# Kernel optimization log

Hardware: AMD Instinct MI355X
Metric: run time of the kernel (lower is better)

## Reference

```python
import jax, jax.numpy as jnp
import numpy as np

B, N, D, H, NCB, TOPK = 4, 2048, 256, 2048, 256, 16
DP = D // 4
SCALE = float(np.sqrt(DP))
THRESH = 0.7
EPS = 1e-8


def setup_inputs() -> dict:
    key = jax.random.key(0)
    ks = jax.random.split(key, 12)
    g = lambda i, shape, s=1.0: jax.random.normal(ks[i], shape, jnp.float32) * s
    return {
        "agent_states": g(0, (B, N, D)),
        "agent_actions": g(1, (B, N, D)),
        "episodic_mem": g(2, (B, N, H)),
        "Wq": g(3, (D, DP), 0.05), "bq": jnp.zeros((DP,), jnp.float32),
        "Wk": g(4, (D, DP), 0.05), "bk": jnp.zeros((DP,), jnp.float32),
        "log_temp": jnp.asarray(0.0, jnp.float32),
        "Wc": g(5, (D, DP), 0.05), "bc": jnp.zeros((DP,), jnp.float32),
        "temp_coal": jnp.asarray(10.0, jnp.float32),
        "W_to_hdc": g(6, (D, H), 0.05), "b_to_hdc": jnp.zeros((H,), jnp.float32),
        "W_from_hdc": g(7, (H, D), 0.02), "b_from_hdc": jnp.zeros((D,), jnp.float32),
        "agent_keys": jnp.sign(g(8, (N, H))),
        "position_codes": jnp.sign(g(9, (NCB, H))),
        "step": 3,
    }


def _cosine(a, b):
    # torch F.cosine_similarity semantics, dim=-1, eps=1e-8
    na = jnp.maximum(jnp.linalg.norm(a, axis=-1), EPS)
    nb = jnp.maximum(jnp.linalg.norm(b, axis=-1), EPS)
    return jnp.sum(a * b, axis=-1) / (na * nb)


def _to_hdc_ste(x):
    soft = jnp.tanh(x * 3.0)
    hard = jnp.sign(x)
    hard = jnp.where(hard == 0, jnp.ones_like(hard), hard)
    return soft + jax.lax.stop_gradient(hard - soft)


def reference(agent_states, agent_actions, episodic_mem, Wq, bq, Wk, bk,
              log_temp, Wc, bc, temp_coal, W_to_hdc, b_to_hdc,
              W_from_hdc, b_from_hdc, agent_keys, position_codes, step):
    # ---- DynamicGraph.compute_graph: top-k dynamic attention adjacency ----
    Q = agent_actions @ Wq + bq                      # (B,N,DP)
    K = agent_actions @ Wk + bk                      # (B,N,DP)
    temp = jnp.clip(jnp.exp(log_temp), 0.1, 10.0)
    scores = jnp.einsum('bnd,bmd->bnm', Q, K) / (SCALE * temp)   # (B,N,N)
    _, topk_idx = jax.lax.top_k(scores, TOPK)                     # (B,N,k)
    bI = jnp.arange(B)[:, None, None]
    nI = jnp.arange(N)[None, :, None]
    mask = jnp.zeros_like(scores).at[bI, nI, topk_idx].set(1.0)   # scatter, like torch scatter_
    scores = scores * mask + (1.0 - mask) * -1e9
    adjacency = jax.nn.softmax(scores, axis=-1)
    # message passing over dynamic graph
    incoming = jnp.einsum('bnm,bmd->bnd', adjacency, agent_states)

    # ---- AgentCombination: sigmoid-normalized coalition mixing ----
    proj = agent_actions @ Wc + bc                   # (B,N,DP)
    pn = proj / jnp.maximum(jnp.linalg.norm(proj, axis=-1, keepdims=True), 1e-12)
    sim = jnp.einsum('bnd,bmd->bnm', pn, pn)
    cw = jax.nn.sigmoid((sim - THRESH) * temp_coal)
    cw = cw / (jnp.sum(cw, axis=-1, keepdims=True) + EPS)
    combined = jnp.einsum('bnm,bmd->bnd', cw, incoming)
    mixed = 0.8 * incoming + 0.2 * combined          # (B,N,D)

    # ---- HDCMemory: bind / write / read with STE ----
    q = _to_hdc_ste(mixed @ W_to_hdc + b_to_hdc)     # (B,N,H) bipolar via STE
    pq = q * agent_keys[None]                        # bind with agent key
    mem = jax.lax.stop_gradient(episodic_mem)        # memory read is detached in original
    pos_code = position_codes[step % NCB]            # (H,)
    new_mem = 0.95 * mem + 0.05 * (q * pos_code)     # write: bind + decay bundle
    strength = jax.nn.sigmoid(_cosine(new_mem, pq))[..., None]   # read similarity
    recall = (new_mem @ W_from_hdc + b_from_hdc) * strength      # (B,N,D)
    return mixed + recall
```

## Files before the change

kernel.cpp:

```cpp
#include <hip/hip_runtime.h>
#include <math.h>

#define BATCH 4
#define NN 2048
#define DD 256
#define HH 2048
#define DP 64
#define KTOP 16

typedef float f32x4 __attribute__((ext_vector_type(4)));
typedef short short8 __attribute__((ext_vector_type(8)));
typedef short short4v __attribute__((ext_vector_type(4)));

__device__ __forceinline__ short f2bf(float x) {
    union { float f; unsigned u; } v; v.f = x;
    unsigned r = v.u + 0x7FFFu + ((v.u >> 16) & 1u);
    return (short)(r >> 16);
}
__device__ __forceinline__ float bf2f(short s) {
    union { unsigned u; float f; } v; v.u = ((unsigned)(unsigned short)s) << 16;
    return v.f;
}

__global__ __launch_bounds__(64) void proj_kernel(
    const float* __restrict__ act,
    const float* __restrict__ Wq, const float* __restrict__ bq,
    const float* __restrict__ Wk, const float* __restrict__ bk,
    const float* __restrict__ Wc, const float* __restrict__ bc,
    float* __restrict__ Qo, float* __restrict__ Ko, short* __restrict__ Pno)
{
    const int row0 = blockIdx.x * 4;
    const int t = threadIdx.x;
    __shared__ float rowbuf[4][DD];
    const float* src = act + (size_t)row0 * DD;
    for (int i = t; i < 4 * DD; i += 64) rowbuf[i >> 8][i & 255] = src[i];
    __syncthreads();

    float q[4], k[4], c[4];
    #pragma unroll
    for (int r = 0; r < 4; ++r) { q[r] = bq[t]; k[r] = bk[t]; c[r] = bc[t]; }

    for (int d = 0; d < DD; ++d) {
        float wq = Wq[d * DP + t];
        float wk = Wk[d * DP + t];
        float wc = Wc[d * DP + t];
        #pragma unroll
        for (int r = 0; r < 4; ++r) {
            float av = rowbuf[r][d];
            q[r] = fmaf(av, wq, q[r]);
            k[r] = fmaf(av, wk, k[r]);
            c[r] = fmaf(av, wc, c[r]);
        }
    }
    #pragma unroll
    for (int r = 0; r < 4; ++r) {
        float ss = c[r] * c[r];
        #pragma unroll
        for (int off = 32; off; off >>= 1) ss += __shfl_xor(ss, off);
        float nrm = fmaxf(sqrtf(ss), 1e-12f);
        size_t o = (size_t)(row0 + r) * DP + t;
        Qo[o] = q[r];
        Ko[o] = k[r];
        Pno[o] = f2bf(c[r] / nrm);
    }
}

__global__ __launch_bounds__(256) void prep_kernel(
    const float* __restrict__ W2h, const float* __restrict__ Wfh,
    short* __restrict__ W2hT_hi, short* __restrict__ W2hT_lo,
    short* __restrict__ WfhT_hi, short* __restrict__ WfhT_lo)
{
    int b = blockIdx.x;
    const float* src; short *dhi, *dlo; int R, C, r0, c0;
    if (b < 512) {
        src = W2h; dhi = W2hT_hi; dlo = W2hT_lo; R = 256; C = 2048;
        r0 = (b >> 6) * 32; c0 = (b & 63) * 32;
    } else {
        b -= 512;
        src = Wfh; dhi = WfhT_hi; dlo = WfhT_lo; R = 2048; C = 256;
        r0 = (b >> 3) * 32; c0 = (b & 7) * 32;
    }
    int tx = threadIdx.x & 31, ty = threadIdx.x >> 5;
    __shared__ float tile[32][33];
    #pragma unroll
    for (int i = 0; i < 4; ++i)
        tile[ty + 8 * i][tx] = src[(size_t)(r0 + ty + 8 * i) * C + c0 + tx];
    __syncthreads();
    #pragma unroll
    for (int i = 0; i < 4; ++i) {
        float v = tile[tx][ty + 8 * i];
        short hi = f2bf(v);
        size_t o = (size_t)(c0 + ty + 8 * i) * R + r0 + tx;
        dhi[o] = hi;
        dlo[o] = f2bf(v - bf2f(hi));
    }
}

__global__ __launch_bounds__(512, 4) void attn_fused_kernel(
    const float* __restrict__ Q, const float* __restrict__ K,
    const float* __restrict__ log_temp,
    const float* __restrict__ states, float* __restrict__ incoming)
{
    const int t = threadIdx.x;
    const int w = t >> 6, l = t & 63;
    const int row = blockIdx.x * 8 + w;
    const int b = row >> 11;

    __shared__ float Ksh[128][68];

    const float temp = fminf(fmaxf(expf(log_temp[0]), 0.1f), 10.0f);
    const float scale = 1.0f / (8.0f * temp);

    const float* Kb = K + (size_t)b * NN * DP;
    const float4* qr4 = (const float4*)(Q + (size_t)row * DP);

    float sc[32];

    for (int ch = 0; ch < 16; ++ch) {
        __syncthreads();
        {
            int r = t >> 2, seg = t & 3;
            const float4* src = (const float4*)(Kb + (size_t)(ch * 128 + r) * DP + seg * 16);
            float4* dst = (float4*)&Ksh[r][seg * 16];
            dst[0] = src[0]; dst[1] = src[1]; dst[2] = src[2]; dst[3] = src[3];
        }
        __syncthreads();
        float a0 = 0.f, a1 = 0.f;
        const float4* k0 = (const float4*)&Ksh[l][0];
        const float4* k1 = (const float4*)&Ksh[64 + l][0];
        #pragma unroll
        for (int h = 0; h < 2; ++h) {
            float4 q[8];
            #pragma unroll
            for (int i = 0; i < 8; ++i) q[i] = qr4[h * 8 + i];
            #pragma unroll
            for (int i = 0; i < 8; ++i) {
                float4 kv0 = k0[h * 8 + i];
                float4 kv1 = k1[h * 8 + i];
                a0 = fmaf(kv0.x, q[i].x, fmaf(kv0.y, q[i].y, fmaf(kv0.z, q[i].z, fmaf(kv0.w, q[i].w, a0))));
                a1 = fmaf(kv1.x, q[i].x, fmaf(kv1.y, q[i].y, fmaf(kv1.z, q[i].z, fmaf(kv1.w, q[i].w, a1))));
            }
        }
        sc[ch * 2]     = a0 * scale;
        sc[ch * 2 + 1] = a1 * scale;
    }

    float wv = 0.f; int wm = 0;
    for (int it = 0; it < KTOP; ++it) {
        float bv = sc[0]; int bs = 0;
        #pragma unroll
        for (int i = 1; i < 32; ++i) {
            bool g = sc[i] > bv;
            bv = g ? sc[i] : bv;
            bs = g ? i : bs;
        }
        int bm = (bs >> 1) * 128 + (bs & 1) * 64 + l;
        #pragma unroll
        for (int off = 1; off < 64; off <<= 1) {
            float ov = __shfl_xor(bv, off);
            int   om = __shfl_xor(bm, off);
            bool take = (ov > bv) || (ov == bv && om < bm);
            bv = take ? ov : bv;
            bm = take ? om : bm;
        }
        if (l == it) { wv = bv; wm = bm; }
        if ((bm & 63) == l) {
            int s = ((bm >> 7) << 1) | ((bm >> 6) & 1);
            #pragma unroll
            for (int i = 0; i < 32; ++i) if (s == i) sc[i] = -3.0e38f;
        }
    }

    float mx = __shfl(wv, 0);
    float e = (l < KTOP) ? expf(wv - mx) : 0.f;
    float Z = e;
    #pragma unroll
    for (int off = 1; off < 64; off <<= 1) Z += __shfl_xor(Z, off);
    float wnorm = e / Z;

    const float* Sb = states + (size_t)b * NN * DD;
    f32x4 acc = (f32x4){0.f, 0.f, 0.f, 0.f};
    #pragma unroll
    for (int kk = 0; kk < KTOP; ++kk) {
        float wk = __shfl(wnorm, kk);
        int   ik = __shfl(wm, kk);
        const float4 v = *(const float4*)(Sb + (size_t)ik * DD + l * 4);
        acc[0] = fmaf(wk, v.x, acc[0]);
        acc[1] = fmaf(wk, v.y, acc[1]);
        acc[2] = fmaf(wk, v.z, acc[2]);
        acc[3] = fmaf(wk, v.w, acc[3]);
    }
    *(float4*)(incoming + (size_t)row * DD + l * 4) = *(float4*)&acc;
}

__global__ __launch_bounds__(256) void coal_kernel(
    const short* __restrict__ pnb_g, const float* __restrict__ incoming,
    const float* __restrict__ temp_coal, float* __restrict__ mixed)
{
    const int b  = blockIdx.x >> 7;
    const int rem = blockIdx.x & 127;
    const int n0 = (rem >> 1) * 32;
    const int dh = rem & 1;
    const int t = threadIdx.x;
    const int w = t >> 6;
    const int l = t & 63;

    __shared__ alignas(16) short pnA[32][72];
    __shared__ alignas(16) short pnB[64][72];
    __shared__ alignas(16) short cwt[32][72];
    __shared__ alignas(16) short incT[128][72];
    __shared__ float rowsum[32];

    const size_t bbase = (size_t)b * NN;

    {
        int r = t >> 3, k8 = (t & 7) * 8;
        *(short8*)&pnA[r][k8] = *(const short8*)(pnb_g + (bbase + n0 + r) * DP + k8);
    }
    if (t < 32) rowsum[t] = 0.0f;

    const float tc = temp_coal[0];

    f32x4 acc[2][2];
    #pragma unroll
    for (int i = 0; i < 2; ++i)
        #pragma unroll
        for (int j = 0; j < 2; ++j)
            acc[i][j] = (f32x4){0.f, 0.f, 0.f, 0.f};

    const int lrow = l & 15;
    const int lk   = (l >> 4) * 8;

    for (int ch = 0; ch < 32; ++ch) {
        const int m0 = ch * 64;
        __syncthreads();

        {
            int r = t >> 2, kq = (t & 3) * 16;
            const short* src = pnb_g + (bbase + m0 + r) * DP + kq;
            *(short8*)&pnB[r][kq]     = *(const short8*)src;
            *(short8*)&pnB[r][kq + 8] = *(const short8*)(src + 8);
        }
        {
            int d4 = t & 31;
            int mg = t >> 5;
            const float* incb = incoming + (bbase + m0) * DD + dh * 128 + d4 * 4;
            #pragma unroll
            for (int i = 0; i < 8; ++i) {
                int m = mg * 8 + i;
                float4 v = *(const float4*)(incb + (size_t)m * DD);
                int db = d4 * 4;
                incT[db + 0][m] = f2bf(v.x);
                incT[db + 1][m] = f2bf(v.y);
                incT[db + 2][m] = f2bf(v.z);
                incT[db + 3][m] = f2bf(v.w);
            }
        }
        __syncthreads();

        f32x4 sacc[2];
        sacc[0] = (f32x4){0.f, 0.f, 0.f, 0.f};
        sacc[1] = (f32x4){0.f, 0.f, 0.f, 0.f};
        #pragma unroll
        for (int ks = 0; ks < 2; ++ks) {
            short8 bfr = *(const short8*)&pnB[w * 16 + lrow][lk + ks * 32];
            short8 a0  = *(const short8*)&pnA[lrow][lk + ks * 32];
            short8 a1  = *(const short8*)&pnA[16 + lrow][lk + ks * 32];
            sacc[0] = __builtin_amdgcn_mfma_f32_16x16x32_bf16(a0, bfr, sacc[0], 0, 0, 0);
            sacc[1] = __builtin_amdgcn_mfma_f32_16x16x32_bf16(a1, bfr, sacc[1], 0, 0, 0);
        }
        #pragma unroll
        for (int rt = 0; rt < 2; ++rt) {
            #pragma unroll
            for (int j = 0; j < 4; ++j) {
                int rr = rt * 16 + (l >> 4) * 4 + j;
                int cc = w * 16 + lrow;
                float cv = 1.0f / (1.0f + expf(-(sacc[rt][j] - 0.7f) * tc));
                cwt[rr][cc] = f2bf(cv);
            }
        }
        __syncthreads();

        {
            int r = t >> 3, c8 = (t & 7) * 8;
            short8 cv = *(const short8*)&cwt[r][c8];
            float p = 0.f;
            #pragma unroll
            for (int j = 0; j < 8; ++j) p += bf2f(cv[j]);
            p += __shfl_xor(p, 1);
            p += __shfl_xor(p, 2);
            p += __shfl_xor(p, 4);
            if ((t & 7) == 0) rowsum[r] += p;
        }

        #pragma unroll
        for (int ks = 0; ks < 2; ++ks) {
            short8 a0 = *(const short8*)&cwt[lrow][lk + ks * 32];
            short8 a1 = *(const short8*)&cwt[16 + lrow][lk + ks * 32];
            #pragma unroll
            for (int ct = 0; ct < 2; ++ct) {
                short8 bfr = *(const short8*)&incT[w * 32 + ct * 16 + lrow][lk + ks * 32];
                acc[0][ct] = __builtin_amdgcn_mfma_f32_16x16x32_bf16(a0, bfr, acc[0][ct], 0, 0, 0);
                acc[1][ct] = __builtin_amdgcn_mfma_f32_16x16x32_bf16(a1, bfr, acc[1][ct], 0, 0, 0);
            }
        }
    }
    __syncthreads();

    #pragma unroll
    for (int rt = 0; rt < 2; ++rt) {
        #pragma unroll
        for (int ct = 0; ct < 2; ++ct) {
            #pragma unroll
            for (int j = 0; j < 4; ++j) {
                int rr = rt * 16 + (l >> 4) * 4 + j;
                int cc = w * 32 + ct * 16 + lrow;
                float inv = 1.0f / (rowsum[rr] + 1e-8f);
                float comb = acc[rt][ct][j] * inv;
                size_t gi = (bbase + n0 + rr) * DD + dh * 128 + cc;
                mixed[gi] = 0.8f * incoming[gi] + 0.2f * comb;
            }
        }
    }
}

__global__ __launch_bounds__(256) void hdcA_kernel(
    const float* __restrict__ mixed,
    const short* __restrict__ W2hT_hi, const short* __restrict__ W2hT_lo,
    const float* __restrict__ b2h,
    unsigned short* __restrict__ qbits)
{
    const int rb = blockIdx.x >> 3;
    const int hs = blockIdx.x & 7;
    const int row0 = rb * 32;
    const int hbase = hs * 256;
    const int t = threadIdx.x;
    const int w = t >> 6, l = t & 63;
    const int lr = l & 15, lg = l >> 4;

    __shared__ short Ahi[32][264], Alo[32][264];
    __shared__ short Whi[64][136], Wlo[64][136];

    #pragma unroll
    for (int i = 0; i < 8; ++i) {
        int idx = t + i * 256;
        int r = idx >> 6, c = (idx & 63) * 4;
        float4 v = *(const float4*)(mixed + (size_t)(row0 + r) * DD + c);
        short4v hi4, lo4;
        hi4[0] = f2bf(v.x); lo4[0] = f2bf(v.x - bf2f(hi4[0]));
        hi4[1] = f2bf(v.y); lo4[1] = f2bf(v.y - bf2f(hi4[1]));
        hi4[2] = f2bf(v.z); lo4[2] = f2bf(v.z - bf2f(hi4[2]));
        hi4[3] = f2bf(v.w); lo4[3] = f2bf(v.w - bf2f(hi4[3]));
        *(short4v*)&Ahi[r][c] = hi4;
        *(short4v*)&Alo[r][c] = lo4;
    }

    for (int ch = 0; ch < 4; ++ch) {
        const int h0 = hbase + ch * 64;
        f32x4 zac[2];
        zac[0] = (f32x4){0.f, 0.f, 0.f, 0.f};
        zac[1] = (f32x4){0.f, 0.f, 0.f, 0.f};
        #pragma unroll
        for (int ks = 0; ks < 2; ++ks) {
            const int k0 = ks * 128;
            __syncthreads();
            {
                int r = t >> 2, cb = (t & 3) * 32;
                const short* sh = W2hT_hi + (size_t)(h0 + r) * DD + k0 + cb;
                const short* sl = W2hT_lo + (size_t)(h0 + r) * DD + k0 + cb;
                #pragma unroll
                for (int j = 0; j < 4; ++j) {
                    *(short8*)&Whi[r][cb + j * 8] = *(const short8*)(sh + j * 8);
                    *(short8*)&Wlo[r][cb + j * 8] = *(const short8*)(sl + j * 8);
                }
            }
            __syncthreads();
            #pragma unroll
            for (int kt = 0; kt < 4; ++kt) {
                int kk = k0 + kt * 32 + lg * 8;
                int kw = kt * 32 + lg * 8;
                short8 bhi = *(const short8*)&Whi[w * 16 + lr][kw];
                short8 blo = *(const short8*)&Wlo[w * 16 + lr][kw];
                #pragma unroll
                for (int mt = 0; mt < 2; ++mt) {
                    short8 ahi = *(const short8*)&Ahi[mt * 16 + lr][kk];
                    short8 alo = *(const short8*)&Alo[mt * 16 + lr][kk];
                    zac[mt] = __builtin_amdgcn_mfma_f32_16x16x32_bf16(ahi, bhi, zac[mt], 0, 0, 0);
                    zac[mt] = __builtin_amdgcn_mfma_f32_16x16x32_bf16(ahi, blo, zac[mt], 0, 0, 0);
                    zac[mt] = __builtin_amdgcn_mfma_f32_16x16x32_bf16(alo, bhi, zac[mt], 0, 0, 0);
                }
            }
        }
        const float bv = b2h[h0 + w * 16 + lr];
        #pragma unroll
        for (int mt = 0; mt < 2; ++mt) {
            #pragma unroll
            for (int j = 0; j < 4; ++j) {
                float z = zac[mt][j] + bv;
                unsigned long long bal = __ballot(z >= 0.0f);
                if (lr == 0)
                    qbits[(size_t)(row0 + mt * 16 + lg * 4 + j) * 128 + (h0 >> 4) + w] =
                        (unsigned short)((bal >> (lg * 16)) & 0xFFFFull);
            }
        }
    }
}

__global__ __launch_bounds__(512) void hdcB_kernel(
    const float* __restrict__ mem, const unsigned short* __restrict__ qbits,
    const float* __restrict__ pos_codes, const int* __restrict__ step,
    const short* __restrict__ WfhT_hi,
    const float* __restrict__ bfh, const float* __restrict__ keys,
    const float* __restrict__ mixed, float* __restrict__ out)
{
    const int mb = blockIdx.x >> 1, nb = blockIdx.x & 1;
    const int row0 = mb * 32, d0 = nb * 128;
    const int t = threadIdx.x;
    const int w = t >> 6, l = t & 63;
    const int wm = w >> 2, wn = w & 3;
    const int lr = l & 15, lg = l >> 4;

    __shared__ short Ahi[32][72], Alo[32][72];
    __shared__ short Bhi[128][72];
    __shared__ float sred[32][2];
    __shared__ float strenL[32];

    int st = ((step[0] % 256) + 256) % 256;
    const float* pos = pos_codes + (size_t)st * HH;

    f32x4 acc[2];
    acc[0] = (f32x4){0.f, 0.f, 0.f, 0.f};
    acc[1] = (f32x4){0.f, 0.f, 0.f, 0.f};
    float pnum = 0.f, pns = 0.f;

    const int ar = t >> 4;
    const int ah = (t & 15) * 4;
    const int arow = row0 + ar;
    const size_t memb = (size_t)arow * HH;
    const size_t keyb = (size_t)(arow & (NN - 1)) * HH;

    for (int kc = 0; kc < 32; ++kc) {
        const int h0 = kc * 64;
        __syncthreads();
        {
            float4 mv = *(const float4*)(mem + memb + h0 + ah);
            float4 kv = *(const float4*)(keys + keyb + h0 + ah);
            float4 pv = *(const float4*)(pos + h0 + ah);
            unsigned bits = (unsigned)qbits[(size_t)arow * 128 + ((h0 + ah) >> 4)] >> (ah & 15);
            float mvs[4] = { mv.x, mv.y, mv.z, mv.w };
            float kvs[4] = { kv.x, kv.y, kv.z, kv.w };
            float pvs[4] = { pv.x, pv.y, pv.z, pv.w };
            short4v hi4, lo4;
            #pragma unroll
            for (int j = 0; j < 4; ++j) {
                float q = ((bits >> j) & 1u) ? 1.0f : -1.0f;
                float nmv = fmaf(0.05f * q, pvs[j], 0.95f * mvs[j]);
                pnum = fmaf(nmv, q * kvs[j], pnum);
                pns  = fmaf(nmv, nmv, pns);
                hi4[j] = f2bf(nmv);
                lo4[j] = f2bf(nmv - bf2f(hi4[j]));
            }
            *(short4v*)&Ahi[ar][ah] = hi4;
            *(short4v*)&Alo[ar][ah] = lo4;
        }
        {
            int r = t >> 2, hb = (t & 3) * 16;
            const short* sh = WfhT_hi + (size_t)(d0 + r) * HH + h0 + hb;
            *(short8*)&Bhi[r][hb]     = *(const short8*)sh;
            *(short8*)&Bhi[r][hb + 8] = *(const short8*)(sh + 8);
        }
        __syncthreads();
        #pragma unroll
        for (int kt = 0; kt < 2; ++kt) {
            const int kk = kt * 32 + lg * 8;
            short8 ahi = *(const short8*)&Ahi[wm * 16 + lr][kk];
            short8 alo = *(const short8*)&Alo[wm * 16 + lr][kk];
            #pragma unroll
            for (int nt = 0; nt < 2; ++nt) {
                short8 bhi = *(const short8*)&Bhi[wn * 32 + nt * 16 + lr][kk];
                acc[nt] = __builtin_amdgcn_mfma_f32_16x16x32_bf16(ahi, bhi, acc[nt], 0, 0, 0);
                acc[nt] = __builtin_amdgcn_mfma_f32_16x16x32_bf16(alo, bhi, acc[nt], 0, 0, 0);
            }
        }
    }

    #pragma unroll
    for (int off = 1; off < 16; off <<= 1) {
        pnum += __shfl_xor(pnum, off);
        pns  += __shfl_xor(pns, off);
    }
    if ((t & 15) == 0) { sred[ar][0] = pnum; sred[ar][1] = pns; }
    __syncthreads();
    if (t < 32) {
        float cosv = sred[t][0] / (fmaxf(sqrtf(sred[t][1]), 1e-8f) * sqrtf(2048.0f));
        strenL[t] = 1.0f / (1.0f + expf(-cosv));
    }
    __syncthreads();

    #pragma unroll
    for (int nt = 0; nt < 2; ++nt) {
        #pragma unroll
        for (int j = 0; j < 4; ++j) {
            int rloc = wm * 16 + lg * 4 + j;
            int col = d0 + wn * 32 + nt * 16 + lr;
            size_t gi = (size_t)(row0 + rloc) * DD + col;
            out[gi] = mixed[gi] + (acc[nt][j] + bfh[col]) * strenL[rloc];
        }
    }
}

extern "C" void kernel_launch(void* const* d_in, const int* in_sizes, int n_in,
                              void* d_out, int out_size, void* d_ws, size_t ws_size,
                              hipStream_t stream) {
    const float* states    = (const float*)d_in[0];
    const float* actions   = (const float*)d_in[1];
    const float* mem       = (const float*)d_in[2];
    const float* Wq        = (const float*)d_in[3];
    const float* bq        = (const float*)d_in[4];
    const float* Wk        = (const float*)d_in[5];
    const float* bk        = (const float*)d_in[6];
    const float* log_temp  = (const float*)d_in[7];
    const float* Wc        = (const float*)d_in[8];
    const float* bc        = (const float*)d_in[9];
    const float* temp_coal = (const float*)d_in[10];
    const float* W2h       = (const float*)d_in[11];
    const float* b2h       = (const float*)d_in[12];
    const float* Wfh       = (const float*)d_in[13];
    const float* bfh       = (const float*)d_in[14];
    const float* keys      = (const float*)d_in[15];
    const float* pos_codes = (const float*)d_in[16];
    const int*   step      = (const int*)d_in[17];
    float* out = (float*)d_out;

    float* ws = (float*)d_ws;
    float* mixed    = ws;
    short* W2hT_hi  = (short*)(mixed + 2097152);
    short* W2hT_lo  = W2hT_hi + 524288;
    short* WfhT_hi  = W2hT_lo + 524288;
    short* WfhT_lo  = WfhT_hi + 524288;
    unsigned short* qbits = (unsigned short*)(WfhT_lo + 524288);
    float* Q        = (float*)(qbits + 1048576);
    float* K        = Q + 524288;
    float* incoming = K + 524288;
    short* pn_bf    = (short*)(incoming + 2097152);

    proj_kernel<<<BATCH * NN / 4, 64, 0, stream>>>(actions, Wq, bq, Wk, bk, Wc, bc, Q, K, pn_bf);
    prep_kernel<<<1024, 256, 0, stream>>>(W2h, Wfh, W2hT_hi, W2hT_lo, WfhT_hi, WfhT_lo);
    attn_fused_kernel<<<BATCH * NN / 8, 512, 0, stream>>>(Q, K, log_temp, states, incoming);
    coal_kernel<<<BATCH * (NN / 32) * 2, 256, 0, stream>>>(pn_bf, incoming, temp_coal, mixed);
    hdcA_kernel<<<(BATCH * NN / 32) * 8, 256, 0, stream>>>(mixed, W2hT_hi, W2hT_lo, b2h, qbits);
    hdcB_kernel<<<(BATCH * NN / 32) * 2, 512, 0, stream>>>(mem, qbits, pos_codes, step,
                                                           WfhT_hi, bfh, keys, mixed, out);
}
```

Before: 338.4 us.

## Compute attention scores with split-bf16 MFMA instead of FP32 FMA loops

Q and K are now stored as three bf16 components (hi/mid/lo), and the score matrix is computed with six 16x16x32 bf16 MFMAs per k-slice, which emulates fp32 precision on matrix cores. K is read straight from global memory rather than staged in shared memory. Scores pass through a small shared buffer so each wave gets its row's 32 values, and the column indexing for top-k is updated to match. The qbits buffer now aliases the Q split storage. This adds two barriers per chunk and uses more memory traffic for the split operands, and top-k ties could differ slightly because of rounding.

```diff
diff --git a/kernel.cpp b/kernel.cpp
--- a/kernel.cpp
+++ b/kernel.cpp
@@ -27,7 +27,9 @@
     const float* __restrict__ Wq, const float* __restrict__ bq,
     const float* __restrict__ Wk, const float* __restrict__ bk,
     const float* __restrict__ Wc, const float* __restrict__ bc,
-    float* __restrict__ Qo, float* __restrict__ Ko, short* __restrict__ Pno)
+    short* __restrict__ Qh, short* __restrict__ Qm, short* __restrict__ Ql,
+    short* __restrict__ Kh, short* __restrict__ Km, short* __restrict__ Kl,
+    short* __restrict__ Pno)
 {
     const int row0 = blockIdx.x * 4;
     const int t = threadIdx.x;
@@ -59,8 +61,12 @@
         for (int off = 32; off; off >>= 1) ss += __shfl_xor(ss, off);
         float nrm = fmaxf(sqrtf(ss), 1e-12f);
         size_t o = (size_t)(row0 + r) * DP + t;
-        Qo[o] = q[r];
-        Ko[o] = k[r];
+        short h1 = f2bf(q[r]); float rs = q[r] - bf2f(h1);
+        short m1 = f2bf(rs);   rs -= bf2f(m1);
+        Qh[o] = h1; Qm[o] = m1; Ql[o] = f2bf(rs);
+        h1 = f2bf(k[r]); rs = k[r] - bf2f(h1);
+        m1 = f2bf(rs);   rs -= bf2f(m1);
+        Kh[o] = h1; Km[o] = m1; Kl[o] = f2bf(rs);
         Pno[o] = f2bf(c[r] / nrm);
     }
 }
@@ -96,53 +102,60 @@
     }
 }
 
-__global__ __launch_bounds__(512, 4) void attn_fused_kernel(
-    const float* __restrict__ Q, const float* __restrict__ K,
+__global__ __launch_bounds__(512) void attn_fused_kernel(
+    const short* __restrict__ Qh, const short* __restrict__ Qm, const short* __restrict__ Ql,
+    const short* __restrict__ Kh, const short* __restrict__ Km, const short* __restrict__ Kl,
     const float* __restrict__ log_temp,
     const float* __restrict__ states, float* __restrict__ incoming)
 {
     const int t = threadIdx.x;
     const int w = t >> 6, l = t & 63;
-    const int row = blockIdx.x * 8 + w;
-    const int b = row >> 11;
-
-    __shared__ float Ksh[128][68];
+    const int lr = l & 15, lg = l >> 4;
+    const int row0 = blockIdx.x * 8;
+    const int b = row0 >> 11;
+    const int row = row0 + w;
+
+    const int cpair = w >> 2;
+    const int tl = w & 3;
+
+    __shared__ float scbuf[2][16][68];
 
     const float temp = fminf(fmaxf(expf(log_temp[0]), 0.1f), 10.0f);
     const float scale = 1.0f / (8.0f * temp);
 
-    const float* Kb = K + (size_t)b * NN * DP;
-    const float4* qr4 = (const float4*)(Q + (size_t)row * DP);
+    const size_t qoff = (size_t)(row0 + lr) * DP;
+    const size_t kbase = (size_t)b * NN * DP;
 
     float sc[32];
 
-    for (int ch = 0; ch < 16; ++ch) {
-        __syncthreads();
-        {
-            int r = t >> 2, seg = t & 3;
-            const float4* src = (const float4*)(Kb + (size_t)(ch * 128 + r) * DP + seg * 16);
-            float4* dst = (float4*)&Ksh[r][seg * 16];
-            dst[0] = src[0]; dst[1] = src[1]; dst[2] = src[2]; dst[3] = src[3];
-        }
-        __syncthreads();
-        float a0 = 0.f, a1 = 0.f;
-        const float4* k0 = (const float4*)&Ksh[l][0];
-        const float4* k1 = (const float4*)&Ksh[64 + l][0];
+    for (int it = 0; it < 16; ++it) {
+        const int ch = it * 2 + cpair;
+        const size_t koff = kbase + (size_t)(ch * 64 + tl * 16 + lr) * DP;
+        f32x4 sacc = (f32x4){0.f, 0.f, 0.f, 0.f};
         #pragma unroll
         for (int h = 0; h < 2; ++h) {
-            float4 q[8];
-            #pragma unroll
-            for (int i = 0; i < 8; ++i) q[i] = qr4[h * 8 + i];
-            #pragma unroll
-            for (int i = 0; i < 8; ++i) {
-                float4 kv0 = k0[h * 8 + i];
-                float4 kv1 = k1[h * 8 + i];
-                a0 = fmaf(kv0.x, q[i].x, fmaf(kv0.y, q[i].y, fmaf(kv0.z, q[i].z, fmaf(kv0.w, q[i].w, a0))));
-                a1 = fmaf(kv1.x, q[i].x, fmaf(kv1.y, q[i].y, fmaf(kv1.z, q[i].z, fmaf(kv1.w, q[i].w, a1))));
-            }
-        }
-        sc[ch * 2]     = a0 * scale;
-        sc[ch * 2 + 1] = a1 * scale;
+            const size_t qa = qoff + h * 32 + lg * 8;
+            const size_t ka = koff + h * 32 + lg * 8;
+            short8 ah = *(const short8*)(Qh + qa);
+            short8 am = *(const short8*)(Qm + qa);
+            short8 al = *(const short8*)(Ql + qa);
+            short8 bh = *(const short8*)(Kh + ka);
+            short8 bm = *(const short8*)(Km + ka);
+            short8 bl = *(const short8*)(Kl + ka);
+            sacc = __builtin_amdgcn_mfma_f32_16x16x32_bf16(ah, bh, sacc, 0, 0, 0);
+            sacc = __builtin_amdgcn_mfma_f32_16x16x32_bf16(ah, bm, sacc, 0, 0, 0);
+            sacc = __builtin_amdgcn_mfma_f32_16x16x32_bf16(am, bh, sacc, 0, 0, 0);
+            sacc = __builtin_amdgcn_mfma_f32_16x16x32_bf16(ah, bl, sacc, 0, 0, 0);
+            sacc = __builtin_amdgcn_mfma_f32_16x16x32_bf16(al, bh, sacc, 0, 0, 0);
+            sacc = __builtin_amdgcn_mfma_f32_16x16x32_bf16(am, bm, sacc, 0, 0, 0);
+        }
+        #pragma unroll
+        for (int j = 0; j < 4; ++j)
+            scbuf[cpair][lg * 4 + j][tl * 16 + lr] = sacc[j];
+        __syncthreads();
+        sc[it * 2]     = scbuf[0][w][l] * scale;
+        sc[it * 2 + 1] = scbuf[1][w][l] * scale;
+        __syncthreads();
     }
 
     float wv = 0.f; int wm = 0;
@@ -154,7 +167,7 @@
             bv = g ? sc[i] : bv;
             bs = g ? i : bs;
         }
-        int bm = (bs >> 1) * 128 + (bs & 1) * 64 + l;
+        int bm = bs * 64 + l;
         #pragma unroll
         for (int off = 1; off < 64; off <<= 1) {
             float ov = __shfl_xor(bv, off);
@@ -165,7 +178,7 @@
         }
         if (l == it) { wv = bv; wm = bm; }
         if ((bm & 63) == l) {
-            int s = ((bm >> 7) << 1) | ((bm >> 6) & 1);
+            int s = bm >> 6;
             #pragma unroll
             for (int i = 0; i < 32; ++i) if (s == i) sc[i] = -3.0e38f;
         }
@@ -538,15 +551,21 @@
     short* W2hT_lo  = W2hT_hi + 524288;
     short* WfhT_hi  = W2hT_lo + 524288;
     short* WfhT_lo  = WfhT_hi + 524288;
-    unsigned short* qbits = (unsigned short*)(WfhT_lo + 524288);
-    float* Q        = (float*)(qbits + 1048576);
-    float* K        = Q + 524288;
-    float* incoming = K + 524288;
+    short* Qh       = WfhT_lo + 524288;
+    short* Qm       = Qh + 524288;
+    short* Ql       = Qm + 524288;
+    short* Kh       = Ql + 524288;
+    short* Km       = Kh + 524288;
+    short* Kl       = Km + 524288;
+    float* incoming = (float*)(Kl + 524288);
     short* pn_bf    = (short*)(incoming + 2097152);
-
-    proj_kernel<<<BATCH * NN / 4, 64, 0, stream>>>(actions, Wq, bq, Wk, bk, Wc, bc, Q, K, pn_bf);
+    unsigned short* qbits = (unsigned short*)Qh;
+
+    proj_kernel<<<BATCH * NN / 4, 64, 0, stream>>>(actions, Wq, bq, Wk, bk, Wc, bc,
+                                                   Qh, Qm, Ql, Kh, Km, Kl, pn_bf);
     prep_kernel<<<1024, 256, 0, stream>>>(W2h, Wfh, W2hT_hi, W2hT_lo, WfhT_hi, WfhT_lo);
-    attn_fused_kernel<<<BATCH * NN / 8, 512, 0, stream>>>(Q, K, log_temp, states, incoming);
+    attn_fused_kernel<<<BATCH * NN / 8, 512, 0, stream>>>(Qh, Qm, Ql, Kh, Km, Kl,
+                                                          log_temp, states, incoming);
     coal_kernel<<<BATCH * (NN / 32) * 2, 256, 0, stream>>>(pn_bf, incoming, temp_coal, mixed);
     hdcA_kernel<<<(BATCH * NN / 32) * 8, 256, 0, stream>>>(mixed, W2hT_hi, W2hT_lo, b2h, qbits);
     hdcB_kernel<<<(BATCH * NN / 32) * 2, 512, 0, stream>>>(mem, qbits, pos_codes, step,
```

Result: slower. 368.2 us (+8.8%).
